# Kernel tuning notes

Hardware: AMD Instinct MI355X
Metric: run time of the kernel (lower is better)

Reference implementation:

```python
import jax, jax.numpy as jnp
import numpy as np

RANK = 4
ALPHA = 4.0
SCALE = ALPHA / RANK


def setup_inputs() -> dict:
    key = jax.random.key(0)
    k1, k2, k3, k4 = jax.random.split(key, 4)
    B, S, H = 4, 2048, 2048
    NH, HD = 16, 128
    x = jax.random.normal(k1, (B, S, H), dtype=jnp.float32)
    W_orig = jax.random.normal(k2, (H, NH, HD), dtype=jnp.float32) * (1.0 / np.sqrt(H))
    A_kernel = jax.random.normal(k3, (H, RANK), dtype=jnp.float32) * (1.0 / RANK)
    # B kernel is zero-init in the module; use small randn so the LoRA path is exercised
    B_kernel = jax.random.normal(k4, (RANK, NH, HD), dtype=jnp.float32) * 0.02
    return {"x": x, "W_orig": W_orig, "A_kernel": A_kernel, "B_kernel": B_kernel}


def reference(x, W_orig, A_kernel, B_kernel):
    # original layer: EinsumDense 'abc,cde->abde'  [B,S,H] x [H,NH,HD] -> [B,S,NH,HD]
    original_output = jnp.einsum('bsc,chd->bshd', x, W_orig)
    # LoRA path: Dense to rank, then EinsumDense back up, scaled
    ax = x @ A_kernel                                   # [B,S,r]
    lora_output = jnp.einsum('bsr,rhd->bshd', ax, B_kernel) * SCALE
    return original_output + lora_output
```

## Files before the change

kernel.cpp:

```cpp
#include <hip/hip_runtime.h>
#include <hip/hip_bf16.h>
#include <cstdint>


using bf16 = __hip_bfloat16;
typedef __attribute__((ext_vector_type(8))) __bf16 bf16x8;
typedef __attribute__((ext_vector_type(4))) float f32x4;

constexpr int Mdim = 8192;
constexpr int Ndim = 2048;
constexpr int Kdim = 2048;
constexpr float SCALE = 1.0f;

constexpr int BM = 256, BN = 256, BK = 64;
constexpr int NT2 = Kdim / (2 * BK);
constexpr int CVT_BLOCKS = (Mdim * Kdim) / (256 * 8);
constexpr int PREP_BLOCKS = (Ndim / 64) * (Kdim / 64);

__device__ __forceinline__ void gload_lds16(const void* g, void* l) {
  __builtin_amdgcn_global_load_lds(
      (const __attribute__((address_space(1))) uint32_t*)g,
      (__attribute__((address_space(3))) uint32_t*)l,
      16, 0, 0);
}

__device__ __forceinline__ uint16_t f2bf(float f) {
  return __bfloat16_as_ushort(__float2bfloat16(f));
}

__global__ void prep_all(const float* __restrict__ X,
                         const float* __restrict__ W,
                         const float* __restrict__ A,
                         const float* __restrict__ Bk,
                         uint16_t* __restrict__ Xb,
                         uint16_t* __restrict__ Wt) {
  __shared__ float tile[64][65];

  if (blockIdx.x < CVT_BLOCKS) {
    const int i = blockIdx.x * blockDim.x + threadIdx.x;
    const float4* Xv = (const float4*)X;
    float4 a = Xv[i * 2 + 0];
    float4 b = Xv[i * 2 + 1];
    uint16_t o[8];
    o[0] = f2bf(a.x); o[1] = f2bf(a.y); o[2] = f2bf(a.z); o[3] = f2bf(a.w);
    o[4] = f2bf(b.x); o[5] = f2bf(b.y); o[6] = f2bf(b.z); o[7] = f2bf(b.w);
    *reinterpret_cast<uint4*>(Xb + (size_t)i * 8) = *reinterpret_cast<uint4*>(o);
  } else {
    const int pid = blockIdx.x - CVT_BLOCKS;
    const int tx = threadIdx.x & 63;
    const int ty = threadIdx.x >> 6;
    const int n0 = (pid & 31) * 64, k0 = (pid >> 5) * 64;

    const int n = n0 + tx;
    const float b0 = Bk[0 * Ndim + n];
    const float b1 = Bk[1 * Ndim + n];
    const float b2 = Bk[2 * Ndim + n];
    const float b3 = Bk[3 * Ndim + n];

    for (int i = ty; i < 64; i += 4) {
      const int k = k0 + i;
      float w = W[(size_t)k * Ndim + n];
      w += SCALE * (A[k * 4 + 0] * b0 + A[k * 4 + 1] * b1 +
                    A[k * 4 + 2] * b2 + A[k * 4 + 3] * b3);
      tile[tx][i] = w;
    }
    __syncthreads();
    for (int i = ty; i < 64; i += 4) {
      Wt[(size_t)(n0 + i) * Kdim + (k0 + tx)] = f2bf(tile[i][tx]);
    }
  }
}

#define FENCE() asm volatile("" ::: "memory")
#define VMW(N)  asm volatile("s_waitcnt vmcnt(" #N ")" ::: "memory")
#define PH()                                                                   \
  do {                                                                         \
    FENCE();                                                                   \
    __builtin_amdgcn_s_barrier();                                              \
    FENCE();                                                                   \
  } while (0)

__global__ __launch_bounds__(512, 2) void gemm_8ph(
    const uint16_t* __restrict__ X, const uint16_t* __restrict__ Wt,
    float* __restrict__ out) {
  __shared__ uint16_t lds[65536];

  const int t = threadIdx.x;
  const int wave = t >> 6, lane = t & 63;
  const int wm = wave >> 2, wn = wave & 3;
  const int l15 = lane & 15, kg = lane >> 4;
  const int sw = l15 & 7;

  const int lid = blockIdx.x;
  const int xcd = lid & 7, loc = lid >> 3;
  const int by = xcd * 4 + (loc & 3);
  const int bx = loc >> 2;
  const int m0 = by * BM, n0 = bx * BN;

  const uint16_t* Ag = X + (size_t)m0 * Kdim;
  const uint16_t* Bg = Wt + (size_t)n0 * Kdim;

  const int r8 = lane >> 3;
  const int gc = (lane & 7) ^ r8;
  const int slot0 = wave * 2, slot1 = slot0 + 1;
  const size_t go0 = (size_t)(slot0 * 8 + r8) * Kdim + gc * 8;
  const size_t go1 = (size_t)(slot1 * 8 + r8) * Kdim + gc * 8;

  int aE[2], bE[2];
#pragma unroll
  for (int s2 = 0; s2 < 2; ++s2) {
    const int p = (s2 * 4 + kg) ^ sw;
    aE[s2] = (wm * 64 + l15) * 64 + p * 8;
    bE[s2] = (wn * 32 + l15) * 64 + p * 8;
  }

#define STAGE_A(buf, h, kt)                                                    \
  do {                                                                         \
    gload_lds16(Ag + go0 + (size_t)(h) * 128 * Kdim + (kt),                    \
                &lds[(buf) * 32768 + (h) * 8192 + slot0 * 512]);               \
    gload_lds16(Ag + go1 + (size_t)(h) * 128 * Kdim + (kt),                    \
                &lds[(buf) * 32768 + (h) * 8192 + slot1 * 512]);               \
  } while (0)
#define STAGE_B(buf, h, kt)                                                    \
  do {                                                                         \
    gload_lds16(Bg + go0 + (size_t)(h) * 128 * Kdim + (kt),                    \
                &lds[(buf) * 32768 + 16384 + (h) * 8192 + slot0 * 512]);       \
    gload_lds16(Bg + go1 + (size_t)(h) * 128 * Kdim + (kt),                    \
                &lds[(buf) * 32768 + 16384 + (h) * 8192 + slot1 * 512]);       \
  } while (0)

  bf16x8 a[4][2], b0[2][2], b1[2][2];
  f32x4 acc[8][4] = {};

#define READ_A(QM, buf)                                                        \
  do {                                                                         \
    _Pragma("unroll") for (int ii = 0; ii < 4; ++ii)                           \
        _Pragma("unroll") for (int s2 = 0; s2 < 2; ++s2)                       \
            a[ii][s2] = *reinterpret_cast<const bf16x8*>(                      \
                &lds[(buf) * 32768 + (QM) * 8192 + ii * 1024 + aE[s2]]);       \
  } while (0)
#define READ_B(QN, buf, dst)                                                   \
  do {                                                                         \
    _Pragma("unroll") for (int jj = 0; jj < 2; ++jj)                           \
        _Pragma("unroll") for (int s2 = 0; s2 < 2; ++s2)                       \
            dst[jj][s2] = *reinterpret_cast<const bf16x8*>(                    \
                &lds[(buf) * 32768 + 16384 + (QN) * 8192 + jj * 1024 +         \
                     bE[s2]]);                                                 \
  } while (0)
#define MMA(QM, QN, barr)                                                      \
  do {                                                                         \
    __builtin_amdgcn_s_setprio(1);                                             \
    _Pragma("unroll") for (int s2 = 0; s2 < 2; ++s2)                           \
        _Pragma("unroll") for (int ii = 0; ii < 4; ++ii)                       \
            _Pragma("unroll") for (int jj = 0; jj < 2; ++jj)                   \
                acc[(QM) * 4 + ii][(QN) * 2 + jj] =                            \
                    __builtin_amdgcn_mfma_f32_16x16x32_bf16(                   \
                        a[ii][s2], barr[jj][s2],                               \
                        acc[(QM) * 4 + ii][(QN) * 2 + jj], 0, 0, 0);           \
    __builtin_amdgcn_s_setprio(0);                                             \
  } while (0)
#define STORE_Q(QM, QN)                                                        \
  do {                                                                         \
    _Pragma("unroll") for (int ii = 0; ii < 4; ++ii) {                         \
      const int mb = m0 + (QM) * 128 + wm * 64 + ii * 16 + kg * 4;             \
      _Pragma("unroll") for (int jj = 0; jj < 2; ++jj) {                       \
        const int n = n0 + (QN) * 128 + wn * 32 + jj * 16 + l15;               \
        _Pragma("unroll") for (int r = 0; r < 4; ++r)                          \
            out[(size_t)(mb + r) * Ndim + n] =                                 \
                acc[(QM) * 4 + ii][(QN) * 2 + jj][r];                          \
      }                                                                        \
    }                                                                          \
  } while (0)

  STAGE_B(0, 0, 0); STAGE_A(0, 0, 0); STAGE_B(0, 1, 0); STAGE_A(0, 1, 0);
  FENCE();
  STAGE_B(1, 0, BK); STAGE_A(1, 0, BK); STAGE_B(1, 1, BK);
  FENCE();
  VMW(6); PH();
  READ_A(0, 0); READ_B(0, 0, b0);
  STAGE_A(1, 1, BK);

#pragma unroll 1
  for (int j = 0; j < NT2 - 1; ++j) {
    const int kn0 = j * 128 + 128;
    const int kn1 = j * 128 + 192;

    PH(); MMA(0, 0, b0); READ_B(1, 0, b1);
    PH(); MMA(0, 1, b1); READ_A(1, 0); STAGE_B(0, 0, kn0);
    PH(); MMA(1, 1, b1); STAGE_A(0, 0, kn0);
    VMW(6); PH(); MMA(1, 0, b0);
    READ_A(0, 1); READ_B(0, 1, b0); STAGE_B(0, 1, kn0);
    PH(); MMA(0, 0, b0); READ_B(1, 1, b1); STAGE_A(0, 1, kn0);
    VMW(8); PH(); MMA(0, 1, b1);
    READ_A(1, 1); STAGE_B(1, 0, kn1); STAGE_A(1, 0, kn1);
    PH(); MMA(1, 1, b1); STAGE_B(1, 1, kn1);
    VMW(6); PH(); MMA(1, 0, b0);
    READ_A(0, 0); READ_B(0, 0, b0); STAGE_A(1, 1, kn1);
  }

  PH(); MMA(0, 0, b0); READ_B(1, 0, b1);
  PH(); MMA(0, 1, b1); READ_A(1, 0);
  PH(); MMA(1, 1, b1);
  VMW(4); PH(); MMA(1, 0, b0); READ_A(0, 1); READ_B(0, 1, b0);
  VMW(0); PH(); MMA(0, 0, b0); READ_B(1, 1, b1); STORE_Q(0, 0);
  PH(); MMA(0, 1, b1); READ_A(1, 1); STORE_Q(0, 1);
  PH(); MMA(1, 1, b1); STORE_Q(1, 1);
  PH(); MMA(1, 0, b0); STORE_Q(1, 0);

#undef STAGE_A
#undef STAGE_B
#undef READ_A
#undef READ_B
#undef MMA
#undef STORE_Q
}

extern "C" void kernel_launch(void* const* d_in, const int* in_sizes, int n_in,
                              void* d_out, int out_size, void* d_ws, size_t ws_size,
                              hipStream_t stream) {
  const float* x  = (const float*)d_in[0];
  const float* W  = (const float*)d_in[1];
  const float* A  = (const float*)d_in[2];
  const float* Bk = (const float*)d_in[3];
  float* out = (float*)d_out;

  uint16_t* Xb = (uint16_t*)d_ws;
  uint16_t* Wt = (uint16_t*)((char*)d_ws + (size_t)Mdim * Kdim * 2);

  prep_all<<<CVT_BLOCKS + PREP_BLOCKS, 256, 0, stream>>>(x, W, A, Bk, Xb, Wt);

  gemm_8ph<<<(Mdim / BM) * (Ndim / BN), 512, 0, stream>>>(Xb, Wt, out);
}
```

Baseline: 190.7 us.

## Restructure GEMM main loop from eight to four barrier phases per iteration

Rewrites the software-pipelined bf16 GEMM loop so each iteration uses four barrier-delimited phases instead of eight. Each phase runs two MFMA quadrants back to back and uses sched_barrier fences to keep LDS reads and global-to-LDS staging interleaved in a fixed order. The change aims to cut barrier overhead and give the MFMA units longer uninterrupted runs, with priority raised around each MFMA group. It also reorders the prefetch stages and waitcnt thresholds, which could expose memory latency or introduce races if the counts are wrong.

```diff
diff --git a/kernel.cpp b/kernel.cpp
--- a/kernel.cpp
+++ b/kernel.cpp
@@ -79,8 +79,9 @@
     __builtin_amdgcn_s_barrier();                                              \
     FENCE();                                                                   \
   } while (0)
-
-__global__ __launch_bounds__(512, 2) void gemm_8ph(
+#define SB() __builtin_amdgcn_sched_barrier(0)
+
+__global__ __launch_bounds__(512, 2) void gemm_4ph(
     const uint16_t* __restrict__ X, const uint16_t* __restrict__ Wt,
     float* __restrict__ out) {
   __shared__ uint16_t lds[65536];
@@ -147,9 +148,8 @@
                 &lds[(buf) * 32768 + 16384 + (QN) * 8192 + jj * 1024 +         \
                      bE[s2]]);                                                 \
   } while (0)
-#define MMA(QM, QN, barr)                                                      \
-  do {                                                                         \
-    __builtin_amdgcn_s_setprio(1);                                             \
+#define MMA16(QM, QN, barr)                                                    \
+  do {                                                                         \
     _Pragma("unroll") for (int s2 = 0; s2 < 2; ++s2)                           \
         _Pragma("unroll") for (int ii = 0; ii < 4; ++ii)                       \
             _Pragma("unroll") for (int jj = 0; jj < 2; ++jj)                   \
@@ -157,7 +157,6 @@
                     __builtin_amdgcn_mfma_f32_16x16x32_bf16(                   \
                         a[ii][s2], barr[jj][s2],                               \
                         acc[(QM) * 4 + ii][(QN) * 2 + jj], 0, 0, 0);           \
-    __builtin_amdgcn_s_setprio(0);                                             \
   } while (0)
 #define STORE_Q(QM, QN)                                                        \
   do {                                                                         \
@@ -174,44 +173,92 @@
 
   STAGE_B(0, 0, 0); STAGE_A(0, 0, 0); STAGE_B(0, 1, 0); STAGE_A(0, 1, 0);
   FENCE();
-  STAGE_B(1, 0, BK); STAGE_A(1, 0, BK); STAGE_B(1, 1, BK);
+  STAGE_B(1, 0, BK); STAGE_A(1, 0, BK);
   FENCE();
-  VMW(6); PH();
-  READ_A(0, 0); READ_B(0, 0, b0);
-  STAGE_A(1, 1, BK);
+  VMW(2);
+  PH();
+  READ_A(0, 0); READ_B(0, 0, b0); READ_B(1, 0, b1);
 
 #pragma unroll 1
   for (int j = 0; j < NT2 - 1; ++j) {
+    const int kt1 = j * 128 + 64;
     const int kn0 = j * 128 + 128;
     const int kn1 = j * 128 + 192;
 
-    PH(); MMA(0, 0, b0); READ_B(1, 0, b1);
-    PH(); MMA(0, 1, b1); READ_A(1, 0); STAGE_B(0, 0, kn0);
-    PH(); MMA(1, 1, b1); STAGE_A(0, 0, kn0);
-    VMW(6); PH(); MMA(1, 0, b0);
-    READ_A(0, 1); READ_B(0, 1, b0); STAGE_B(0, 1, kn0);
-    PH(); MMA(0, 0, b0); READ_B(1, 1, b1); STAGE_A(0, 1, kn0);
-    VMW(8); PH(); MMA(0, 1, b1);
-    READ_A(1, 1); STAGE_B(1, 0, kn1); STAGE_A(1, 0, kn1);
-    PH(); MMA(1, 1, b1); STAGE_B(1, 1, kn1);
-    VMW(6); PH(); MMA(1, 0, b0);
-    READ_A(0, 0); READ_B(0, 0, b0); STAGE_A(1, 1, kn1);
-  }
-
-  PH(); MMA(0, 0, b0); READ_B(1, 0, b1);
-  PH(); MMA(0, 1, b1); READ_A(1, 0);
-  PH(); MMA(1, 1, b1);
-  VMW(4); PH(); MMA(1, 0, b0); READ_A(0, 1); READ_B(0, 1, b0);
-  VMW(0); PH(); MMA(0, 0, b0); READ_B(1, 1, b1); STORE_Q(0, 0);
-  PH(); MMA(0, 1, b1); READ_A(1, 1); STORE_Q(0, 1);
-  PH(); MMA(1, 1, b1); STORE_Q(1, 1);
-  PH(); MMA(1, 0, b0); STORE_Q(1, 0);
+    VMW(2); PH();
+    __builtin_amdgcn_s_setprio(1);
+    MMA16(0, 0, b0); SB(); MMA16(0, 1, b1);
+    __builtin_amdgcn_s_setprio(0); SB();
+    READ_A(1, 0); SB();
+    STAGE_B(1, 1, kt1); STAGE_A(1, 1, kt1);
+
+    VMW(1); PH();
+    __builtin_amdgcn_s_setprio(1);
+    MMA16(1, 1, b1); SB();
+    READ_B(1, 1, b1); SB();
+    MMA16(1, 0, b0);
+    __builtin_amdgcn_s_setprio(0); SB();
+    READ_A(0, 1); READ_B(0, 1, b0); SB();
+    STAGE_B(0, 0, kn0); STAGE_A(0, 0, kn0);
+
+    VMW(2); PH();
+    __builtin_amdgcn_s_setprio(1);
+    MMA16(0, 0, b0); SB(); MMA16(0, 1, b1);
+    __builtin_amdgcn_s_setprio(0); SB();
+    READ_A(1, 1); SB();
+    STAGE_B(0, 1, kn0); STAGE_A(0, 1, kn0);
+
+    VMW(1); PH();
+    __builtin_amdgcn_s_setprio(1);
+    MMA16(1, 1, b1); SB();
+    READ_B(1, 0, b1); SB();
+    MMA16(1, 0, b0);
+    __builtin_amdgcn_s_setprio(0); SB();
+    READ_A(0, 0); READ_B(0, 0, b0); SB();
+    STAGE_B(1, 0, kn1); STAGE_A(1, 0, kn1);
+  }
+
+  {
+    const int kt1 = (NT2 - 1) * 128 + 64;
+
+    VMW(2); PH();
+    __builtin_amdgcn_s_setprio(1);
+    MMA16(0, 0, b0); SB(); MMA16(0, 1, b1);
+    __builtin_amdgcn_s_setprio(0); SB();
+    READ_A(1, 0); SB();
+    STAGE_B(1, 1, kt1); STAGE_A(1, 1, kt1);
+
+    VMW(1); PH();
+    __builtin_amdgcn_s_setprio(1);
+    MMA16(1, 1, b1); SB();
+    READ_B(1, 1, b1); SB();
+    MMA16(1, 0, b0);
+    __builtin_amdgcn_s_setprio(0); SB();
+    READ_A(0, 1); READ_B(0, 1, b0); SB();
+
+    VMW(0); PH();
+    __builtin_amdgcn_s_setprio(1);
+    MMA16(0, 0, b0); SB(); MMA16(0, 1, b1);
+    __builtin_amdgcn_s_setprio(0); SB();
+    READ_A(1, 1); SB();
+    STORE_Q(0, 0); STORE_Q(0, 1);
+
+    PH();
+    __builtin_amdgcn_s_setprio(1);
+    MMA16(1, 1, b1);
+    __builtin_amdgcn_s_setprio(0); SB();
+    STORE_Q(1, 1);
+    __builtin_amdgcn_s_setprio(1);
+    MMA16(1, 0, b0);
+    __builtin_amdgcn_s_setprio(0); SB();
+    STORE_Q(1, 0);
+  }
 
 #undef STAGE_A
 #undef STAGE_B
 #undef READ_A
 #undef READ_B
-#undef MMA
+#undef MMA16
 #undef STORE_Q
 }
 
@@ -229,5 +276,5 @@
 
   prep_all<<<CVT_BLOCKS + PREP_BLOCKS, 256, 0, stream>>>(x, W, A, Bk, Xb, Wt);
 
-  gemm_8ph<<<(Mdim / BM) * (Ndim / BN), 512, 0, stream>>>(Xb, Wt, out);
-}
+  gemm_4ph<<<(Mdim / BM) * (Ndim / BN), 512, 0, stream>>>(Xb, Wt, out);
+}
```

After: 208.8 us. 1.1x slower.
